# Kernel optimization log

Hardware: AMD Instinct MI355X
Metric: run time of the kernel (lower is better)

The kernel has to match this reference:

```python
import jax, jax.numpy as jnp
import numpy as np

DIM = 1024
HEADS = 16
HEAD_DIM = DIM // HEADS
B, N = 4, 4096


def setup_inputs() -> dict:
    key = jax.random.key(0)
    ks = jax.random.split(key, 10)
    s = 1.0 / np.sqrt(DIM)
    return {
        "x": jax.random.normal(ks[0], (B, N, DIM), dtype=jnp.float32),
        "Wq": jax.random.uniform(ks[1], (DIM, DIM), jnp.float32, -s, s),
        "bq": jax.random.uniform(ks[2], (DIM,), jnp.float32, -s, s),
        "Wk": jax.random.uniform(ks[3], (DIM, DIM), jnp.float32, -s, s),
        "bk": jax.random.uniform(ks[4], (DIM,), jnp.float32, -s, s),
        "Wv": jax.random.uniform(ks[5], (DIM, DIM), jnp.float32, -s, s),
        "bv": jax.random.uniform(ks[6], (DIM,), jnp.float32, -s, s),
        "Wo": jax.random.uniform(ks[7], (DIM, DIM), jnp.float32, -s, s),
        "bo": jax.random.uniform(ks[8], (DIM,), jnp.float32, -s, s),
        "stdp": jnp.ones((HEADS,), dtype=jnp.float32),
    }


def reference(x, Wq, bq, Wk, bk, Wv, bv, Wo, bo, stdp):
    b, n, d = x.shape
    h, dh = HEADS, HEAD_DIM
    # projections (torch Linear: x @ W.T + b)
    def proj(W, bias):
        return (x @ W.T + bias).reshape(b, n, h, dh).transpose(0, 2, 1, 3)  # bhnd
    Q = jax.nn.elu(proj(Wq, bq)) + 1.0
    K = jax.nn.elu(proj(Wk, bk)) + 1.0
    V = proj(Wv, bv)
    stdp_w = jax.nn.sigmoid(stdp).reshape(1, h, 1, 1)
    KV = jnp.einsum('bhnd,bhnv->bhdv', K, V)      # (b,h,dh,dh)
    K_sum = K.sum(axis=2)                          # (b,h,dh)
    numerator = jnp.einsum('bhnd,bhdv->bhnv', Q, KV)
    denominator = jnp.einsum('bhnd,bhd->bhn', Q, K_sum)[..., None] + 1e-6
    attn_out = numerator / denominator * stdp_w    # (b,h,n,dh)
    out = attn_out.transpose(0, 2, 1, 3).reshape(b, n, d)
    out = out @ Wo.T + bo
    return (out, jax.lax.stop_gradient(stdp))
```

## Files before the change

kernel.cpp:

```cpp
#include <hip/hip_runtime.h>
#include <hip/hip_bf16.h>

#define DIMSZ 1024
#define SEQLEN 4096
#define NHEAD 16
#define NX 16777216L
#define NW 1048576L

typedef __attribute__((ext_vector_type(8))) short bf16x8;
typedef __attribute__((ext_vector_type(4))) float f32x4;

__device__ __forceinline__ unsigned short f2bf(float f) {
    union { float f; unsigned int i; } c; c.f = f;
    unsigned int x = c.i;
    unsigned int r = (x + 0x7fffu + ((x >> 16) & 1u)) >> 16;
    return (unsigned short)r;
}

__device__ __forceinline__ unsigned int pk2(float lo, float hi) {
    union { float f; unsigned int i; } a, b; a.f = lo; b.f = hi;
    return __builtin_amdgcn_perm(b.i + 0x8000u, a.i + 0x8000u, 0x07060302u);
}

__device__ __forceinline__ void unp8r(bf16x8 v, float* f) {
    union { bf16x8 s; uint4 w; } u; u.s = v;
    union { unsigned int i; float f; } c;
    c.i = u.w.x << 16;           f[0] = c.f;
    c.i = u.w.x & 0xffff0000u;   f[1] = c.f;
    c.i = u.w.y << 16;           f[2] = c.f;
    c.i = u.w.y & 0xffff0000u;   f[3] = c.f;
    c.i = u.w.z << 16;           f[4] = c.f;
    c.i = u.w.z & 0xffff0000u;   f[5] = c.f;
    c.i = u.w.w << 16;           f[6] = c.f;
    c.i = u.w.w & 0xffff0000u;   f[7] = c.f;
}

__device__ __forceinline__ void async16(const void* g, void* l) {
    __builtin_amdgcn_global_load_lds(
        (const __attribute__((address_space(1))) void*)g,
        (__attribute__((address_space(3))) void*)l,
        16, 0, 0);
}

__global__ __launch_bounds__(256) void cast_pack(
    const float* __restrict__ x, const float* __restrict__ Wq,
    const float* __restrict__ Wk, const float* __restrict__ Wv,
    const float* __restrict__ Wo, const float* __restrict__ stdp,
    unsigned short* __restrict__ xb, unsigned short* __restrict__ Wqkv,
    unsigned short* __restrict__ Wob, float* __restrict__ outTail)
{
    long i4 = ((long)blockIdx.x * 256 + threadIdx.x) * 4;
    const float* src; unsigned short* dst; long off;
    if (i4 < NX)               { src = x;  dst = xb;          off = i4; }
    else if (i4 < NX + NW)     { src = Wq; dst = Wqkv;        off = i4 - NX; }
    else if (i4 < NX + 2*NW)   { src = Wk; dst = Wqkv + NW;   off = i4 - NX - NW; }
    else if (i4 < NX + 3*NW)   { src = Wv; dst = Wqkv + 2*NW; off = i4 - NX - 2*NW; }
    else                       { src = Wo; dst = Wob;         off = i4 - NX - 3*NW; }
    float4 v = *(const float4*)(src + off);
    union { unsigned short u[4]; uint2 p; } o;
    o.u[0] = f2bf(v.x); o.u[1] = f2bf(v.y); o.u[2] = f2bf(v.z); o.u[3] = f2bf(v.w);
    *(uint2*)(dst + off) = o.p;
    if (blockIdx.x == 0 && threadIdx.x < NHEAD) outTail[threadIdx.x] = stdp[threadIdx.x];
}

__global__ __launch_bounds__(512, 2) void qkv_gemm8(
    const unsigned short* __restrict__ A, const unsigned short* __restrict__ W,
    const float* __restrict__ bq, const float* __restrict__ bk,
    const float* __restrict__ bv,
    unsigned short* __restrict__ Qb, unsigned short* __restrict__ Kb,
    unsigned short* __restrict__ Vb)
{
    __shared__ __align__(16) char SM[131072];
    const int t = threadIdx.x;
    const int wave = t >> 6, lane = t & 63;
    const int lr = lane & 15, lq = lane >> 4;
    const int wm = wave >> 2, wn = wave & 3;
    const int m0 = blockIdx.x * 256;
    const int c0 = blockIdx.y * 256;

    const int sc = (((t & 7) ^ ((t >> 3) & 7)) * 8);
    const unsigned short* pA = A + (long)(m0 + (t >> 3)) * DIMSZ + sc;
    const unsigned short* pB = W + (long)(c0 + (t >> 3)) * DIMSZ + sc;
    char* ldsW = SM + wave * 1024;

    const int xo = ((lq ^ (lr & 7)) << 4);
    const char* ABase = SM + wm * 16384 + lr * 128;
    const char* BBase = SM + 32768 + (wn * 64 + lr) * 128;

    f32x4 acc[8][4];
    #pragma unroll
    for (int i = 0; i < 8; ++i)
        #pragma unroll
        for (int j = 0; j < 4; ++j) acc[i][j] = (f32x4){0.f, 0.f, 0.f, 0.f};

#define STAGE(Q, O) do {                                                        \
        if ((Q) < 16) {                                                         \
            const int isB_ = ((O) < 2) ? 1 : 0;                                 \
            const int half_ = isB_ ? (O) : ((O) - 2);                           \
            const unsigned short* s_ = (isB_ ? pB : pA)                         \
                                       + (long)half_ * 131072 + (Q) * 64;       \
            char* d_ = ldsW + (((Q) & 1) << 16) + isB_ * 32768 + half_ * 16384; \
            async16(s_, d_);                                                    \
            async16(s_ + 65536, d_ + 8192);                                     \
        }                                                                       \
    } while (0)

    STAGE(0, 0); STAGE(0, 1); STAGE(0, 2); STAGE(0, 3);
    STAGE(1, 0); STAGE(1, 1); STAGE(1, 2);
    asm volatile("s_waitcnt vmcnt(6)" ::: "memory");
    __builtin_amdgcn_s_barrier();

    for (int kt = 0; kt < 16; ++kt) {
        const int buf = (kt & 1) << 16;
        bf16x8 a0[4][2], a1[4][2], bfr[4][2];

        #pragma unroll
        for (int j = 0; j < 2; ++j) {
            bfr[j][0] = *(const bf16x8*)(BBase + buf + j * 2048 + xo);
            bfr[j][1] = *(const bf16x8*)(BBase + buf + j * 2048 + (xo ^ 64));
        }
        #pragma unroll
        for (int i = 0; i < 4; ++i) {
            a0[i][0] = *(const bf16x8*)(ABase + buf + i * 2048 + xo);
            a0[i][1] = *(const bf16x8*)(ABase + buf + i * 2048 + (xo ^ 64));
        }
        STAGE(kt + 1, 3);
        __builtin_amdgcn_s_barrier();
        asm volatile("s_waitcnt lgkmcnt(0)" ::: "memory");
        __builtin_amdgcn_sched_barrier(0);
        __builtin_amdgcn_s_setprio(1);
        #pragma unroll
        for (int s = 0; s < 2; ++s)
            #pragma unroll
            for (int i = 0; i < 4; ++i)
                #pragma unroll
                for (int j = 0; j < 2; ++j)
                    acc[i][j] = __builtin_amdgcn_mfma_f32_16x16x32_bf16(
                        bfr[j][s], a0[i][s], acc[i][j], 0, 0, 0);
        __builtin_amdgcn_s_setprio(0);
        __builtin_amdgcn_s_barrier();

        #pragma unroll
        for (int j = 2; j < 4; ++j) {
            bfr[j][0] = *(const bf16x8*)(BBase + buf + j * 2048 + xo);
            bfr[j][1] = *(const bf16x8*)(BBase + buf + j * 2048 + (xo ^ 64));
        }
        __builtin_amdgcn_s_barrier();
        asm volatile("s_waitcnt lgkmcnt(0)" ::: "memory");
        __builtin_amdgcn_sched_barrier(0);
        __builtin_amdgcn_s_setprio(1);
        #pragma unroll
        for (int s = 0; s < 2; ++s)
            #pragma unroll
            for (int i = 0; i < 4; ++i)
                #pragma unroll
                for (int j = 2; j < 4; ++j)
                    acc[i][j] = __builtin_amdgcn_mfma_f32_16x16x32_bf16(
                        bfr[j][s], a0[i][s], acc[i][j], 0, 0, 0);
        __builtin_amdgcn_s_setprio(0);
        __builtin_amdgcn_s_barrier();

        #pragma unroll
        for (int i = 0; i < 4; ++i) {
            a1[i][0] = *(const bf16x8*)(ABase + buf + (i + 4) * 2048 + xo);
            a1[i][1] = *(const bf16x8*)(ABase + buf + (i + 4) * 2048 + (xo ^ 64));
        }
        STAGE(kt + 2, 0);
        __builtin_amdgcn_s_barrier();
        asm volatile("s_waitcnt lgkmcnt(0)" ::: "memory");
        __builtin_amdgcn_sched_barrier(0);
        __builtin_amdgcn_s_setprio(1);
        #pragma unroll
        for (int s = 0; s < 2; ++s)
            #pragma unroll
            for (int i = 0; i < 4; ++i)
                #pragma unroll
                for (int j = 0; j < 2; ++j)
                    acc[i + 4][j] = __builtin_amdgcn_mfma_f32_16x16x32_bf16(
                        bfr[j][s], a1[i][s], acc[i + 4][j], 0, 0, 0);
        __builtin_amdgcn_s_setprio(0);
        __builtin_amdgcn_s_barrier();

        STAGE(kt + 2, 1);
        STAGE(kt + 2, 2);
        __builtin_amdgcn_s_barrier();
        __builtin_amdgcn_s_setprio(1);
        #pragma unroll
        for (int s = 0; s < 2; ++s)
            #pragma unroll
            for (int i = 0; i < 4; ++i)
                #pragma unroll
                for (int j = 2; j < 4; ++j)
                    acc[i + 4][j] = __builtin_amdgcn_mfma_f32_16x16x32_bf16(
                        bfr[j][s], a1[i][s], acc[i + 4][j], 0, 0, 0);
        __builtin_amdgcn_s_setprio(0);
        if (kt < 14)       asm volatile("s_waitcnt vmcnt(6)" ::: "memory");
        else if (kt == 14) asm volatile("s_waitcnt vmcnt(0)" ::: "memory");
        __builtin_amdgcn_s_barrier();
    }
#undef STAGE

    const int proj = c0 >> 10;
    const float* bias = proj == 0 ? bq : (proj == 1 ? bk : bv);
    const bool qk = proj < 2;
    const int cb = (c0 & 1023) + wn * 64;
    const int q4 = lq * 4;
    #pragma unroll
    for (int j = 0; j < 4; ++j) {
        const float4 b4 = *(const float4*)(bias + cb + 16 * j + q4);
        #pragma unroll
        for (int i = 0; i < 8; ++i) {
            float v0 = acc[i][j][0] + b4.x, v1 = acc[i][j][1] + b4.y;
            float v2 = acc[i][j][2] + b4.z, v3 = acc[i][j][3] + b4.w;
            if (qk) {
                v0 = v0 > 0.f ? v0 + 1.f : __expf(v0);
                v1 = v1 > 0.f ? v1 + 1.f : __expf(v1);
                v2 = v2 > 0.f ? v2 + 1.f : __expf(v2);
                v3 = v3 > 0.f ? v3 + 1.f : __expf(v3);
            }
            const int row = wm * 128 + 16 * i + lr;
            int byte = row * 512 + wn * 128 + j * 32 + q4 * 2;
            byte ^= (row & 7) << 4;
            uint2 pkd; pkd.x = pk2(v0, v1); pkd.y = pk2(v2, v3);
            *(uint2*)(SM + byte) = pkd;
        }
    }
    __syncthreads();
    unsigned short* dstp = proj == 0 ? Qb : (proj == 1 ? Kb : Vb);
    const int colsh = (t & 31) * 8;
    const int h = ((c0 >> 6) + (colsh >> 6)) & 15;
    const int b_ = m0 >> 12;
    unsigned short* dbase = dstp + ((long)(b_ * 16 + h) * SEQLEN) * 64 + (colsh & 63);
    #pragma unroll
    for (int u = 0; u < 16; ++u) {
        const int flat = u * 8192 + t * 16;
        const int row = flat >> 9;
        uint4 val = *(const uint4*)(SM + (flat ^ ((row & 7) << 4)));
        const int n = (m0 + row) & 4095;
        *(uint4*)(dbase + (long)n * 64) = val;
    }
}

__global__ __launch_bounds__(256) void kv_reduce(
    const unsigned short* __restrict__ Kb, const unsigned short* __restrict__ Vb,
    float* __restrict__ KVp, float* __restrict__ Ksump)
{
    __shared__ __align__(16) char LDS[65536];
    int bh = blockIdx.x, split = blockIdx.y, t = threadIdx.x;
    int wave = t >> 6, lane = t & 63, lr = lane & 15, lq = lane >> 4;

    const unsigned short* Kbase = Kb + ((long)bh * SEQLEN + split * 256) * 64;
    const unsigned short* Vbase = Vb + ((long)bh * SEQLEN + split * 256) * 64;

    const int nl = t & 127;
    const int dh = (t >> 7) * 32;

    union Q2S { uint4 q[4]; unsigned short s[32]; };
    Q2S kq[2], vq[2];
    #pragma unroll
    for (int it = 0; it < 2; ++it) {
        const unsigned short* kp = Kbase + (long)(it * 128 + nl) * 64 + dh;
        const unsigned short* vp = Vbase + (long)(it * 128 + nl) * 64 + dh;
        #pragma unroll
        for (int g = 0; g < 4; ++g) {
            kq[it].q[g] = *(const uint4*)(kp + g * 8);
            vq[it].q[g] = *(const uint4*)(vp + g * 8);
        }
    }
    #pragma unroll
    for (int it = 0; it < 2; ++it) {
        char* buf = LDS + it * 32768;
        #pragma unroll
        for (int e = 0; e < 32; ++e) {
            const int d = dh + e;
            const int a = d * 256 + ((nl * 2) ^ ((d & 7) << 4));
            *(unsigned short*)(buf + a) = kq[it].s[e];
            *(unsigned short*)(buf + 16384 + a) = vq[it].s[e];
        }
    }
    __syncthreads();

    f32x4 acc[4];
    #pragma unroll
    for (int j = 0; j < 4; ++j) acc[j] = (f32x4){0.f, 0.f, 0.f, 0.f};
    float ksp[4] = {0.f, 0.f, 0.f, 0.f};

    const int vrow = 16 * wave + lr;
    #pragma unroll
    for (int it = 0; it < 2; ++it) {
        const char* buf = LDS + it * 32768;
        #pragma unroll
        for (int ns = 0; ns < 4; ++ns) {
            const int xoff = (ns * 64 + lq * 16) ^ ((lr & 7) << 4);
            bf16x8 af = *(const bf16x8*)(buf + 16384 + vrow * 256 + xoff);
            bf16x8 bfr[4];
            #pragma unroll
            for (int j = 0; j < 4; ++j)
                bfr[j] = *(const bf16x8*)(buf + (16 * j + lr) * 256 + xoff);
            if (wave == 0) {
                #pragma unroll
                for (int j = 0; j < 4; ++j) {
                    float kf[8]; unp8r(bfr[j], kf);
                    ksp[j] += ((kf[0] + kf[1]) + (kf[2] + kf[3]))
                            + ((kf[4] + kf[5]) + (kf[6] + kf[7]));
                }
            }
            #pragma unroll
            for (int j = 0; j < 4; ++j)
                acc[j] = __builtin_amdgcn_mfma_f32_16x16x32_bf16(bfr[j], af, acc[j], 0, 0, 0);
        }
    }

    float* kp = KVp + ((long)split * 64 + bh) * 4096;
    const int q4 = lq * 4;
    #pragma unroll
    for (int j = 0; j < 4; ++j)
        *(f32x4*)(kp + vrow * 64 + 16 * j + q4) = acc[j];

    if (wave == 0) {
        #pragma unroll
        for (int j = 0; j < 4; ++j) {
            float s = ksp[j];
            s += __shfl_xor(s, 16);
            s += __shfl_xor(s, 32);
            if (lane < 16)
                Ksump[((long)split * 64 + bh) * 64 + 16 * j + lr] = s;
        }
    }
}

__global__ __launch_bounds__(256) void kv_final(
    const float* __restrict__ KVp, const float* __restrict__ Ksump,
    unsigned short* __restrict__ KVb, float* __restrict__ Ksum)
{
    int bh = blockIdx.x, t = threadIdx.x;
    float s[16];
    #pragma unroll
    for (int g = 0; g < 16; ++g) s[g] = 0.f;
    for (int sp = 0; sp < 16; ++sp) {
        const float* src = KVp + ((long)sp * 64 + bh) * 4096 + t * 16;
        #pragma unroll
        for (int g = 0; g < 4; ++g) {
            float4 v = *(const float4*)(src + g * 4);
            s[g * 4 + 0] += v.x; s[g * 4 + 1] += v.y;
            s[g * 4 + 2] += v.z; s[g * 4 + 3] += v.w;
        }
    }
    uint4 o0, o1;
    o0.x = pk2(s[0], s[1]);  o0.y = pk2(s[2], s[3]);
    o0.z = pk2(s[4], s[5]);  o0.w = pk2(s[6], s[7]);
    o1.x = pk2(s[8], s[9]);  o1.y = pk2(s[10], s[11]);
    o1.z = pk2(s[12], s[13]); o1.w = pk2(s[14], s[15]);
    *(uint4*)(KVb + (long)bh * 4096 + t * 16) = o0;
    *(uint4*)(KVb + (long)bh * 4096 + t * 16 + 8) = o1;
    if (t < 16) {
        float4 a = {0.f, 0.f, 0.f, 0.f};
        for (int p = 0; p < 16; p += 4) {
            #pragma unroll
            for (int q = 0; q < 4; ++q) {
                float4 v = *(const float4*)(Ksump + ((long)(p + q) * 64 + bh) * 64 + t * 4);
                a.x += v.x; a.y += v.y; a.z += v.z; a.w += v.w;
            }
        }
        *(float4*)(Ksum + bh * 64 + t * 4) = a;
    }
}

__global__ __launch_bounds__(256) void attn_kernel(
    const unsigned short* __restrict__ Qb, const unsigned short* __restrict__ KVb,
    const float* __restrict__ Ksum, const float* __restrict__ stdp,
    unsigned short* __restrict__ attn)
{
    __shared__ unsigned short Cs[256 * 72];
    int t = threadIdx.x;
    int rc = blockIdx.x;
    int bh = blockIdx.y;
    int b = bh >> 4, h = bh & 15;

    int wave = t >> 6, lane = t & 63, lr = lane & 15, lk = (lane >> 4) * 8;
    int rowbase = rc * 256 + wave * 64;
    const unsigned short* kvb = KVb + (long)bh * 4096;
    const float* ksb = Ksum + bh * 64;

    f32x4 acc[4][4];
    #pragma unroll
    for (int i = 0; i < 4; ++i)
        #pragma unroll
        for (int j = 0; j < 4; ++j) acc[i][j] = (f32x4){0.f, 0.f, 0.f, 0.f};
    float ds[4] = {0.f, 0.f, 0.f, 0.f};

    #pragma unroll
    for (int s0 = 0; s0 < 64; s0 += 32) {
        bf16x8 af[4], bfr[4];
        #pragma unroll
        for (int i = 0; i < 4; ++i)
            af[i] = *(const bf16x8*)(Qb + ((long)bh * SEQLEN + rowbase + 16 * i + lr) * 64 + s0 + lk);
        #pragma unroll
        for (int j = 0; j < 4; ++j)
            bfr[j] = *(const bf16x8*)(kvb + (16 * j + lr) * 64 + s0 + lk);
        float4 ka = *(const float4*)(ksb + s0 + lk);
        float4 kb2 = *(const float4*)(ksb + s0 + lk + 4);
        float ksf[8] = {ka.x, ka.y, ka.z, ka.w, kb2.x, kb2.y, kb2.z, kb2.w};
        #pragma unroll
        for (int i = 0; i < 4; ++i) {
            float qf[8]; unp8r(af[i], qf);
            #pragma unroll
            for (int e = 0; e < 8; ++e) ds[i] += qf[e] * ksf[e];
        }
        #pragma unroll
        for (int i = 0; i < 4; ++i)
            #pragma unroll
            for (int j = 0; j < 4; ++j)
                acc[i][j] = __builtin_amdgcn_mfma_f32_16x16x32_bf16(bfr[j], af[i], acc[i][j], 0, 0, 0);
    }

    float sg = 1.f / (1.f + __expf(-stdp[h]));
    float dinv_i[4];
    #pragma unroll
    for (int i = 0; i < 4; ++i) {
        float d = ds[i];
        d += __shfl_xor(d, 16);
        d += __shfl_xor(d, 32);
        dinv_i[i] = sg / (d + 1e-6f);
    }

    int q4 = (lane >> 4) * 4;
    #pragma unroll
    for (int j = 0; j < 4; ++j) {
        int v0c = 16 * j + q4;
        #pragma unroll
        for (int i = 0; i < 4; ++i) {
            int row = wave * 64 + 16 * i + lr;
            float d = dinv_i[i];
            uint2 pkd;
            pkd.x = pk2(acc[i][j][0] * d, acc[i][j][1] * d);
            pkd.y = pk2(acc[i][j][2] * d, acc[i][j][3] * d);
            *(uint2*)(Cs + row * 72 + v0c) = pkd;
        }
    }
    __syncthreads();
    #pragma unroll
    for (int u = 0; u < 8; ++u) {
        int row = u * 32 + (t >> 3);
        int nn = rc * 256 + row;
        long a = ((long)(b * SEQLEN + nn)) * DIMSZ + h * 64 + (t & 7) * 8;
        *(uint4*)(attn + a) = *(const uint4*)(Cs + row * 72 + (t & 7) * 8);
    }
}

__global__ __launch_bounds__(512, 2) void out_gemm8(
    const unsigned short* __restrict__ A, const unsigned short* __restrict__ W,
    const float* __restrict__ bo, float* __restrict__ out)
{
    __shared__ __align__(16) char SM[131072];
    const int t = threadIdx.x;
    const int wave = t >> 6, lane = t & 63;
    const int lr = lane & 15, lq = lane >> 4;
    const int wm = wave >> 2, wn = wave & 3;
    const int m0 = blockIdx.x * 256;
    const int c0 = blockIdx.y * 256;

    const int sc = (((t & 7) ^ ((t >> 3) & 7)) * 8);
    const unsigned short* pA = A + (long)(m0 + (t >> 3)) * DIMSZ + sc;
    const unsigned short* pB = W + (long)(c0 + (t >> 3)) * DIMSZ + sc;
    char* ldsW = SM + wave * 1024;

    const int xo = ((lq ^ (lr & 7)) << 4);
    const char* ABase = SM + wm * 16384 + lr * 128;
    const char* BBase = SM + 32768 + (wn * 64 + lr) * 128;

    f32x4 acc[8][4];
    #pragma unroll
    for (int i = 0; i < 8; ++i)
        #pragma unroll
        for (int j = 0; j < 4; ++j) acc[i][j] = (f32x4){0.f, 0.f, 0.f, 0.f};

#define STAGE(Q, O) do {                                                        \
        if ((Q) < 16) {                                                         \
            const int isB_ = ((O) < 2) ? 1 : 0;                                 \
            const int half_ = isB_ ? (O) : ((O) - 2);                           \
            const unsigned short* s_ = (isB_ ? pB : pA)                         \
                                       + (long)half_ * 131072 + (Q) * 64;       \
            char* d_ = ldsW + (((Q) & 1) << 16) + isB_ * 32768 + half_ * 16384; \
            async16(s_, d_);                                                    \
            async16(s_ + 65536, d_ + 8192);                                     \
        }                                                                       \
    } while (0)

    STAGE(0, 0); STAGE(0, 1); STAGE(0, 2); STAGE(0, 3);
    STAGE(1, 0); STAGE(1, 1); STAGE(1, 2);
    asm volatile("s_waitcnt vmcnt(6)" ::: "memory");
    __builtin_amdgcn_s_barrier();

    for (int kt = 0; kt < 16; ++kt) {
        const int buf = (kt & 1) << 16;
        bf16x8 a0[4][2], a1[4][2], bfr[4][2];

        #pragma unroll
        for (int j = 0; j < 2; ++j) {
            bfr[j][0] = *(const bf16x8*)(BBase + buf + j * 2048 + xo);
            bfr[j][1] = *(const bf16x8*)(BBase + buf + j * 2048 + (xo ^ 64));
        }
        #pragma unroll
        for (int i = 0; i < 4; ++i) {
            a0[i][0] = *(const bf16x8*)(ABase + buf + i * 2048 + xo);
            a0[i][1] = *(const bf16x8*)(ABase + buf + i * 2048 + (xo ^ 64));
        }
        STAGE(kt + 1, 3);
        __builtin_amdgcn_s_barrier();
        asm volatile("s_waitcnt lgkmcnt(0)" ::: "memory");
        __builtin_amdgcn_sched_barrier(0);
        __builtin_amdgcn_s_setprio(1);
        #pragma unroll
        for (int s = 0; s < 2; ++s)
            #pragma unroll
            for (int i = 0; i < 4; ++i)
                #pragma unroll
                for (int j = 0; j < 2; ++j)
                    acc[i][j] = __builtin_amdgcn_mfma_f32_16x16x32_bf16(
                        bfr[j][s], a0[i][s], acc[i][j], 0, 0, 0);
        __builtin_amdgcn_s_setprio(0);
        __builtin_amdgcn_s_barrier();

        #pragma unroll
        for (int j = 2; j < 4; ++j) {
            bfr[j][0] = *(const bf16x8*)(BBase + buf + j * 2048 + xo);
            bfr[j][1] = *(const bf16x8*)(BBase + buf + j * 2048 + (xo ^ 64));
        }
        __builtin_amdgcn_s_barrier();
        asm volatile("s_waitcnt lgkmcnt(0)" ::: "memory");
        __builtin_amdgcn_sched_barrier(0);
        __builtin_amdgcn_s_setprio(1);
        #pragma unroll
        for (int s = 0; s < 2; ++s)
            #pragma unroll
            for (int i = 0; i < 4; ++i)
                #pragma unroll
                for (int j = 2; j < 4; ++j)
                    acc[i][j] = __builtin_amdgcn_mfma_f32_16x16x32_bf16(
                        bfr[j][s], a0[i][s], acc[i][j], 0, 0, 0);
        __builtin_amdgcn_s_setprio(0);
        __builtin_amdgcn_s_barrier();

        #pragma unroll
        for (int i = 0; i < 4; ++i) {
            a1[i][0] = *(const bf16x8*)(ABase + buf + (i + 4) * 2048 + xo);
            a1[i][1] = *(const bf16x8*)(ABase + buf + (i + 4) * 2048 + (xo ^ 64));
        }
        STAGE(kt + 2, 0);
        __builtin_amdgcn_s_barrier();
        asm volatile("s_waitcnt lgkmcnt(0)" ::: "memory");
        __builtin_amdgcn_sched_barrier(0);
        __builtin_amdgcn_s_setprio(1);
        #pragma unroll
        for (int s = 0; s < 2; ++s)
            #pragma unroll
            for (int i = 0; i < 4; ++i)
                #pragma unroll
                for (int j = 0; j < 2; ++j)
                    acc[i + 4][j] = __builtin_amdgcn_mfma_f32_16x16x32_bf16(
                        bfr[j][s], a1[i][s], acc[i + 4][j], 0, 0, 0);
        __builtin_amdgcn_s_setprio(0);
        __builtin_amdgcn_s_barrier();

        STAGE(kt + 2, 1);
        STAGE(kt + 2, 2);
        __builtin_amdgcn_s_barrier();
        __builtin_amdgcn_s_setprio(1);
        #pragma unroll
        for (int s = 0; s < 2; ++s)
            #pragma unroll
            for (int i = 0; i < 4; ++i)
                #pragma unroll
                for (int j = 2; j < 4; ++j)
                    acc[i + 4][j] = __builtin_amdgcn_mfma_f32_16x16x32_bf16(
                        bfr[j][s], a1[i][s], acc[i + 4][j], 0, 0, 0);
        __builtin_amdgcn_s_setprio(0);
        if (kt < 14)       asm volatile("s_waitcnt vmcnt(6)" ::: "memory");
        else if (kt == 14) asm volatile("s_waitcnt vmcnt(0)" ::: "memory");
        __builtin_amdgcn_s_barrier();
    }
#undef STAGE

    const int q4 = lq * 4;
    #pragma unroll
    for (int j = 0; j < 4; ++j) {
        const int c = c0 + wn * 64 + 16 * j + q4;
        const float4 b4 = *(const float4*)(bo + c);
        #pragma unroll
        for (int i = 0; i < 8; ++i) {
            const int gm = m0 + wm * 128 + 16 * i + lr;
            float4 v;
            v.x = acc[i][j][0] + b4.x; v.y = acc[i][j][1] + b4.y;
            v.z = acc[i][j][2] + b4.z; v.w = acc[i][j][3] + b4.w;
            *(float4*)(out + (long)gm * DIMSZ + c) = v;
        }
    }
}

extern "C" void kernel_launch(void* const* d_in, const int* in_sizes, int n_in,
                              void* d_out, int out_size, void* d_ws, size_t ws_size,
                              hipStream_t stream) {
    const float* x    = (const float*)d_in[0];
    const float* Wq   = (const float*)d_in[1];
    const float* bq   = (const float*)d_in[2];
    const float* Wk   = (const float*)d_in[3];
    const float* bk   = (const float*)d_in[4];
    const float* Wv   = (const float*)d_in[5];
    const float* bv   = (const float*)d_in[6];
    const float* Wo   = (const float*)d_in[7];
    const float* bo   = (const float*)d_in[8];
    const float* stdp = (const float*)d_in[9];
    float* out = (float*)d_out;

    char* ws = (char*)d_ws;
    unsigned short* xb   = (unsigned short*)(ws);
    float*          KVp  = (float*)(ws);
    unsigned short* attn = (unsigned short*)(ws);
    unsigned short* Wqkv = (unsigned short*)(ws + 33554432L);
    float*          Ksump= (float*)(ws + 33554432L);
    unsigned short* KVb  = (unsigned short*)(ws + 33816576L);
    float*          Ksum = (float*)(ws + 34340864L);
    unsigned short* Wob  = (unsigned short*)(ws + 39845888L);
    unsigned short* Qb   = (unsigned short*)(ws + 41943040L);
    unsigned short* Kb   = (unsigned short*)(ws + 75497472L);
    unsigned short* Vb   = (unsigned short*)(ws + 109051904L);

    cast_pack<<<20480, 256, 0, stream>>>(x, Wq, Wk, Wv, Wo, stdp, xb, Wqkv, Wob,
                                         out + 16777216L);
    qkv_gemm8<<<dim3(64, 12), 512, 0, stream>>>(xb, Wqkv, bq, bk, bv, Qb, Kb, Vb);
    kv_reduce<<<dim3(64, 16), 256, 0, stream>>>(Kb, Vb, KVp, Ksump);
    kv_final<<<64, 256, 0, stream>>>(KVp, Ksump, KVb, Ksum);
    attn_kernel<<<dim3(16, 64), 256, 0, stream>>>(Qb, KVb, Ksum, stdp, attn);
    out_gemm8<<<dim3(64, 4), 512, 0, stream>>>(attn, Wob, bo, out);
}
```

Before: 323.8 us.

## Reschedule GEMM LDS loads, halve KV-reduce splits, and double attention rows per block

Both GEMM main loops now load all four B fragments up front and redistribute the global-to-LDS staging calls across phases, removing one barrier/wait pair per k-step. The KV reduction processes two 256-row chunks per block with half as many splits, so the final reduce sums fewer partials. The attention kernel keeps KV and Ksum fragments in registers and handles two row chunks per block, halving the grid. This trades register pressure and less parallelism for fewer barriers, less redundant loading and lower launch overhead.

```diff
diff --git a/kernel.cpp b/kernel.cpp
--- a/kernel.cpp
+++ b/kernel.cpp
@@ -6,6 +6,7 @@
 #define NHEAD 16
 #define NX 16777216L
 #define NW 1048576L
+#define KVSPLITS 8
 
 typedef __attribute__((ext_vector_type(8))) short bf16x8;
 typedef __attribute__((ext_vector_type(4))) float f32x4;
@@ -115,7 +116,7 @@
         bf16x8 a0[4][2], a1[4][2], bfr[4][2];
 
         #pragma unroll
-        for (int j = 0; j < 2; ++j) {
+        for (int j = 0; j < 4; ++j) {
             bfr[j][0] = *(const bf16x8*)(BBase + buf + j * 2048 + xo);
             bfr[j][1] = *(const bf16x8*)(BBase + buf + j * 2048 + (xo ^ 64));
         }
@@ -125,6 +126,7 @@
             a0[i][1] = *(const bf16x8*)(ABase + buf + i * 2048 + (xo ^ 64));
         }
         STAGE(kt + 1, 3);
+        asm volatile("s_waitcnt lgkmcnt(8)" ::: "memory");
         __builtin_amdgcn_s_barrier();
         asm volatile("s_waitcnt lgkmcnt(0)" ::: "memory");
         __builtin_amdgcn_sched_barrier(0);
@@ -140,14 +142,8 @@
         __builtin_amdgcn_s_setprio(0);
         __builtin_amdgcn_s_barrier();
 
-        #pragma unroll
-        for (int j = 2; j < 4; ++j) {
-            bfr[j][0] = *(const bf16x8*)(BBase + buf + j * 2048 + xo);
-            bfr[j][1] = *(const bf16x8*)(BBase + buf + j * 2048 + (xo ^ 64));
-        }
-        __builtin_amdgcn_s_barrier();
-        asm volatile("s_waitcnt lgkmcnt(0)" ::: "memory");
-        __builtin_amdgcn_sched_barrier(0);
+        STAGE(kt + 2, 0);
+        __builtin_amdgcn_s_barrier();
         __builtin_amdgcn_s_setprio(1);
         #pragma unroll
         for (int s = 0; s < 2; ++s)
@@ -165,7 +161,7 @@
             a1[i][0] = *(const bf16x8*)(ABase + buf + (i + 4) * 2048 + xo);
             a1[i][1] = *(const bf16x8*)(ABase + buf + (i + 4) * 2048 + (xo ^ 64));
         }
-        STAGE(kt + 2, 0);
+        STAGE(kt + 2, 1);
         __builtin_amdgcn_s_barrier();
         asm volatile("s_waitcnt lgkmcnt(0)" ::: "memory");
         __builtin_amdgcn_sched_barrier(0);
@@ -181,7 +177,6 @@
         __builtin_amdgcn_s_setprio(0);
         __builtin_amdgcn_s_barrier();
 
-        STAGE(kt + 2, 1);
         STAGE(kt + 2, 2);
         __builtin_amdgcn_s_barrier();
         __builtin_amdgcn_s_setprio(1);
@@ -249,65 +244,68 @@
     int bh = blockIdx.x, split = blockIdx.y, t = threadIdx.x;
     int wave = t >> 6, lane = t & 63, lr = lane & 15, lq = lane >> 4;
 
-    const unsigned short* Kbase = Kb + ((long)bh * SEQLEN + split * 256) * 64;
-    const unsigned short* Vbase = Vb + ((long)bh * SEQLEN + split * 256) * 64;
-
     const int nl = t & 127;
     const int dh = (t >> 7) * 32;
-
-    union Q2S { uint4 q[4]; unsigned short s[32]; };
-    Q2S kq[2], vq[2];
-    #pragma unroll
-    for (int it = 0; it < 2; ++it) {
-        const unsigned short* kp = Kbase + (long)(it * 128 + nl) * 64 + dh;
-        const unsigned short* vp = Vbase + (long)(it * 128 + nl) * 64 + dh;
-        #pragma unroll
-        for (int g = 0; g < 4; ++g) {
-            kq[it].q[g] = *(const uint4*)(kp + g * 8);
-            vq[it].q[g] = *(const uint4*)(vp + g * 8);
-        }
-    }
-    #pragma unroll
-    for (int it = 0; it < 2; ++it) {
-        char* buf = LDS + it * 32768;
-        #pragma unroll
-        for (int e = 0; e < 32; ++e) {
-            const int d = dh + e;
-            const int a = d * 256 + ((nl * 2) ^ ((d & 7) << 4));
-            *(unsigned short*)(buf + a) = kq[it].s[e];
-            *(unsigned short*)(buf + 16384 + a) = vq[it].s[e];
-        }
-    }
-    __syncthreads();
+    const int vrow = 16 * wave + lr;
 
     f32x4 acc[4];
     #pragma unroll
     for (int j = 0; j < 4; ++j) acc[j] = (f32x4){0.f, 0.f, 0.f, 0.f};
     float ksp[4] = {0.f, 0.f, 0.f, 0.f};
 
-    const int vrow = 16 * wave + lr;
-    #pragma unroll
-    for (int it = 0; it < 2; ++it) {
-        const char* buf = LDS + it * 32768;
-        #pragma unroll
-        for (int ns = 0; ns < 4; ++ns) {
-            const int xoff = (ns * 64 + lq * 16) ^ ((lr & 7) << 4);
-            bf16x8 af = *(const bf16x8*)(buf + 16384 + vrow * 256 + xoff);
-            bf16x8 bfr[4];
-            #pragma unroll
-            for (int j = 0; j < 4; ++j)
-                bfr[j] = *(const bf16x8*)(buf + (16 * j + lr) * 256 + xoff);
-            if (wave == 0) {
-                #pragma unroll
-                for (int j = 0; j < 4; ++j) {
-                    float kf[8]; unp8r(bfr[j], kf);
-                    ksp[j] += ((kf[0] + kf[1]) + (kf[2] + kf[3]))
-                            + ((kf[4] + kf[5]) + (kf[6] + kf[7]));
+    for (int half = 0; half < 2; ++half) {
+        const unsigned short* Kbase = Kb + ((long)bh * SEQLEN + split * 512 + half * 256) * 64;
+        const unsigned short* Vbase = Vb + ((long)bh * SEQLEN + split * 512 + half * 256) * 64;
+
+        union Q2S { uint4 q[4]; unsigned short s[32]; };
+        Q2S kq[2], vq[2];
+        #pragma unroll
+        for (int it = 0; it < 2; ++it) {
+            const unsigned short* kp = Kbase + (long)(it * 128 + nl) * 64 + dh;
+            const unsigned short* vp = Vbase + (long)(it * 128 + nl) * 64 + dh;
+            #pragma unroll
+            for (int g = 0; g < 4; ++g) {
+                kq[it].q[g] = *(const uint4*)(kp + g * 8);
+                vq[it].q[g] = *(const uint4*)(vp + g * 8);
+            }
+        }
+        if (half) __syncthreads();
+        #pragma unroll
+        for (int it = 0; it < 2; ++it) {
+            char* buf = LDS + it * 32768;
+            #pragma unroll
+            for (int e = 0; e < 32; ++e) {
+                const int d = dh + e;
+                const int a = d * 256 + ((nl * 2) ^ ((d & 7) << 4));
+                *(unsigned short*)(buf + a) = kq[it].s[e];
+                *(unsigned short*)(buf + 16384 + a) = vq[it].s[e];
+            }
+        }
+        __syncthreads();
+
+        #pragma unroll
+        for (int it = 0; it < 2; ++it) {
+            const char* buf = LDS + it * 32768;
+            #pragma unroll
+            for (int ns = 0; ns < 4; ++ns) {
+                const int xoff = (ns * 64 + lq * 16) ^ ((lr & 7) << 4);
+                bf16x8 af = *(const bf16x8*)(buf + 16384 + vrow * 256 + xoff);
+                bf16x8 bfr[4];
+                #pragma unroll
+                for (int j = 0; j < 4; ++j)
+                    bfr[j] = *(const bf16x8*)(buf + (16 * j + lr) * 256 + xoff);
+                if (wave == 0) {
+                    #pragma unroll
+                    for (int j = 0; j < 4; ++j) {
+                        float kf[8]; unp8r(bfr[j], kf);
+                        ksp[j] += ((kf[0] + kf[1]) + (kf[2] + kf[3]))
+                                + ((kf[4] + kf[5]) + (kf[6] + kf[7]));
+                    }
                 }
+                #pragma unroll
+                for (int j = 0; j < 4; ++j)
+                    acc[j] = __builtin_amdgcn_mfma_f32_16x16x32_bf16(bfr[j], af, acc[j], 0, 0, 0);
             }
-            #pragma unroll
-            for (int j = 0; j < 4; ++j)
-                acc[j] = __builtin_amdgcn_mfma_f32_16x16x32_bf16(bfr[j], af, acc[j], 0, 0, 0);
         }
     }
 
@@ -337,7 +335,7 @@
     float s[16];
     #pragma unroll
     for (int g = 0; g < 16; ++g) s[g] = 0.f;
-    for (int sp = 0; sp < 16; ++sp) {
+    for (int sp = 0; sp < KVSPLITS; ++sp) {
         const float* src = KVp + ((long)sp * 64 + bh) * 4096 + t * 16;
         #pragma unroll
         for (int g = 0; g < 4; ++g) {
@@ -355,7 +353,7 @@
     *(uint4*)(KVb + (long)bh * 4096 + t * 16 + 8) = o1;
     if (t < 16) {
         float4 a = {0.f, 0.f, 0.f, 0.f};
-        for (int p = 0; p < 16; p += 4) {
+        for (int p = 0; p < KVSPLITS; p += 4) {
             #pragma unroll
             for (int q = 0; q < 4; ++q) {
                 float4 v = *(const float4*)(Ksump + ((long)(p + q) * 64 + bh) * 64 + t * 4);
@@ -373,78 +371,89 @@
 {
     __shared__ unsigned short Cs[256 * 72];
     int t = threadIdx.x;
-    int rc = blockIdx.x;
     int bh = blockIdx.y;
     int b = bh >> 4, h = bh & 15;
 
     int wave = t >> 6, lane = t & 63, lr = lane & 15, lk = (lane >> 4) * 8;
-    int rowbase = rc * 256 + wave * 64;
     const unsigned short* kvb = KVb + (long)bh * 4096;
     const float* ksb = Ksum + bh * 64;
 
-    f32x4 acc[4][4];
-    #pragma unroll
-    for (int i = 0; i < 4; ++i)
-        #pragma unroll
-        for (int j = 0; j < 4; ++j) acc[i][j] = (f32x4){0.f, 0.f, 0.f, 0.f};
-    float ds[4] = {0.f, 0.f, 0.f, 0.f};
-
-    #pragma unroll
-    for (int s0 = 0; s0 < 64; s0 += 32) {
-        bf16x8 af[4], bfr[4];
+    bf16x8 bfrh[2][4];
+    float ksf[2][8];
+    #pragma unroll
+    for (int s = 0; s < 2; ++s) {
+        #pragma unroll
+        for (int j = 0; j < 4; ++j)
+            bfrh[s][j] = *(const bf16x8*)(kvb + (16 * j + lr) * 64 + s * 32 + lk);
+        float4 ka = *(const float4*)(ksb + s * 32 + lk);
+        float4 kb2 = *(const float4*)(ksb + s * 32 + lk + 4);
+        ksf[s][0] = ka.x; ksf[s][1] = ka.y; ksf[s][2] = ka.z; ksf[s][3] = ka.w;
+        ksf[s][4] = kb2.x; ksf[s][5] = kb2.y; ksf[s][6] = kb2.z; ksf[s][7] = kb2.w;
+    }
+    float sg = 1.f / (1.f + __expf(-stdp[h]));
+    int q4 = (lane >> 4) * 4;
+
+    for (int c = 0; c < 2; ++c) {
+        int rc = blockIdx.x * 2 + c;
+        int rowbase = rc * 256 + wave * 64;
+
+        f32x4 acc[4][4];
         #pragma unroll
         for (int i = 0; i < 4; ++i)
-            af[i] = *(const bf16x8*)(Qb + ((long)bh * SEQLEN + rowbase + 16 * i + lr) * 64 + s0 + lk);
-        #pragma unroll
-        for (int j = 0; j < 4; ++j)
-            bfr[j] = *(const bf16x8*)(kvb + (16 * j + lr) * 64 + s0 + lk);
-        float4 ka = *(const float4*)(ksb + s0 + lk);
-        float4 kb2 = *(const float4*)(ksb + s0 + lk + 4);
-        float ksf[8] = {ka.x, ka.y, ka.z, ka.w, kb2.x, kb2.y, kb2.z, kb2.w};
+            #pragma unroll
+            for (int j = 0; j < 4; ++j) acc[i][j] = (f32x4){0.f, 0.f, 0.f, 0.f};
+        float ds[4] = {0.f, 0.f, 0.f, 0.f};
+
+        #pragma unroll
+        for (int s = 0; s < 2; ++s) {
+            bf16x8 af[4];
+            #pragma unroll
+            for (int i = 0; i < 4; ++i)
+                af[i] = *(const bf16x8*)(Qb + ((long)bh * SEQLEN + rowbase + 16 * i + lr) * 64 + s * 32 + lk);
+            #pragma unroll
+            for (int i = 0; i < 4; ++i) {
+                float qf[8]; unp8r(af[i], qf);
+                #pragma unroll
+                for (int e = 0; e < 8; ++e) ds[i] += qf[e] * ksf[s][e];
+            }
+            #pragma unroll
+            for (int i = 0; i < 4; ++i)
+                #pragma unroll
+                for (int j = 0; j < 4; ++j)
+                    acc[i][j] = __builtin_amdgcn_mfma_f32_16x16x32_bf16(bfrh[s][j], af[i], acc[i][j], 0, 0, 0);
+        }
+
+        float dinv_i[4];
         #pragma unroll
         for (int i = 0; i < 4; ++i) {
-            float qf[8]; unp8r(af[i], qf);
-            #pragma unroll
-            for (int e = 0; e < 8; ++e) ds[i] += qf[e] * ksf[e];
-        }
-        #pragma unroll
-        for (int i = 0; i < 4; ++i)
-            #pragma unroll
-            for (int j = 0; j < 4; ++j)
-                acc[i][j] = __builtin_amdgcn_mfma_f32_16x16x32_bf16(bfr[j], af[i], acc[i][j], 0, 0, 0);
-    }
-
-    float sg = 1.f / (1.f + __expf(-stdp[h]));
-    float dinv_i[4];
-    #pragma unroll
-    for (int i = 0; i < 4; ++i) {
-        float d = ds[i];
-        d += __shfl_xor(d, 16);
-        d += __shfl_xor(d, 32);
-        dinv_i[i] = sg / (d + 1e-6f);
-    }
-
-    int q4 = (lane >> 4) * 4;
-    #pragma unroll
-    for (int j = 0; j < 4; ++j) {
-        int v0c = 16 * j + q4;
-        #pragma unroll
-        for (int i = 0; i < 4; ++i) {
-            int row = wave * 64 + 16 * i + lr;
-            float d = dinv_i[i];
-            uint2 pkd;
-            pkd.x = pk2(acc[i][j][0] * d, acc[i][j][1] * d);
-            pkd.y = pk2(acc[i][j][2] * d, acc[i][j][3] * d);
-            *(uint2*)(Cs + row * 72 + v0c) = pkd;
-        }
-    }
-    __syncthreads();
-    #pragma unroll
-    for (int u = 0; u < 8; ++u) {
-        int row = u * 32 + (t >> 3);
-        int nn = rc * 256 + row;
-        long a = ((long)(b * SEQLEN + nn)) * DIMSZ + h * 64 + (t & 7) * 8;
-        *(uint4*)(attn + a) = *(const uint4*)(Cs + row * 72 + (t & 7) * 8);
+            float d = ds[i];
+            d += __shfl_xor(d, 16);
+            d += __shfl_xor(d, 32);
+            dinv_i[i] = sg / (d + 1e-6f);
+        }
+
+        #pragma unroll
+        for (int j = 0; j < 4; ++j) {
+            int v0c = 16 * j + q4;
+            #pragma unroll
+            for (int i = 0; i < 4; ++i) {
+                int row = wave * 64 + 16 * i + lr;
+                float d = dinv_i[i];
+                uint2 pkd;
+                pkd.x = pk2(acc[i][j][0] * d, acc[i][j][1] * d);
+                pkd.y = pk2(acc[i][j][2] * d, acc[i][j][3] * d);
+                *(uint2*)(Cs + row * 72 + v0c) = pkd;
+            }
+        }
+        __syncthreads();
+        #pragma unroll
+        for (int u = 0; u < 8; ++u) {
+            int row = u * 32 + (t >> 3);
+            int nn = rc * 256 + row;
+            long a = ((long)(b * SEQLEN + nn)) * DIMSZ + h * 64 + (t & 7) * 8;
+            *(uint4*)(attn + a) = *(const uint4*)(Cs + row * 72 + (t & 7) * 8);
+        }
+        __syncthreads();
     }
 }
 
@@ -497,7 +506,7 @@
         bf16x8 a0[4][2], a1[4][2], bfr[4][2];
 
         #pragma unroll
-        for (int j = 0; j < 2; ++j) {
+        for (int j = 0; j < 4; ++j) {
             bfr[j][0] = *(const bf16x8*)(BBase + buf + j * 2048 + xo);
             bfr[j][1] = *(const bf16x8*)(BBase + buf + j * 2048 + (xo ^ 64));
         }
@@ -507,6 +516,7 @@
             a0[i][1] = *(const bf16x8*)(ABase + buf + i * 2048 + (xo ^ 64));
         }
         STAGE(kt + 1, 3);
+        asm volatile("s_waitcnt lgkmcnt(8)" ::: "memory");
         __builtin_amdgcn_s_barrier();
         asm volatile("s_waitcnt lgkmcnt(0)" ::: "memory");
         __builtin_amdgcn_sched_barrier(0);
@@ -522,14 +532,8 @@
         __builtin_amdgcn_s_setprio(0);
         __builtin_amdgcn_s_barrier();
 
-        #pragma unroll
-        for (int j = 2; j < 4; ++j) {
-            bfr[j][0] = *(const bf16x8*)(BBase + buf + j * 2048 + xo);
-            bfr[j][1] = *(const bf16x8*)(BBase + buf + j * 2048 + (xo ^ 64));
-        }
-        __builtin_amdgcn_s_barrier();
-        asm volatile("s_waitcnt lgkmcnt(0)" ::: "memory");
-        __builtin_amdgcn_sched_barrier(0);
+        STAGE(kt + 2, 0);
+        __builtin_amdgcn_s_barrier();
         __builtin_amdgcn_s_setprio(1);
         #pragma unroll
         for (int s = 0; s < 2; ++s)
@@ -547,7 +551,7 @@
             a1[i][0] = *(const bf16x8*)(ABase + buf + (i + 4) * 2048 + xo);
             a1[i][1] = *(const bf16x8*)(ABase + buf + (i + 4) * 2048 + (xo ^ 64));
         }
-        STAGE(kt + 2, 0);
+        STAGE(kt + 2, 1);
         __builtin_amdgcn_s_barrier();
         asm volatile("s_waitcnt lgkmcnt(0)" ::: "memory");
         __builtin_amdgcn_sched_barrier(0);
@@ -563,7 +567,6 @@
         __builtin_amdgcn_s_setprio(0);
         __builtin_amdgcn_s_barrier();
 
-        STAGE(kt + 2, 1);
         STAGE(kt + 2, 2);
         __builtin_amdgcn_s_barrier();
         __builtin_amdgcn_s_setprio(1);
@@ -629,8 +632,8 @@
     cast_pack<<<20480, 256, 0, stream>>>(x, Wq, Wk, Wv, Wo, stdp, xb, Wqkv, Wob,
                                          out + 16777216L);
     qkv_gemm8<<<dim3(64, 12), 512, 0, stream>>>(xb, Wqkv, bq, bk, bv, Qb, Kb, Vb);
-    kv_reduce<<<dim3(64, 16), 256, 0, stream>>>(Kb, Vb, KVp, Ksump);
+    kv_reduce<<<dim3(64, KVSPLITS), 256, 0, stream>>>(Kb, Vb, KVp, Ksump);
     kv_final<<<64, 256, 0, stream>>>(KVp, Ksump, KVb, Ksum);
-    attn_kernel<<<dim3(16, 64), 256, 0, stream>>>(Qb, KVb, Ksum, stdp, attn);
+    attn_kernel<<<dim3(8, 64), 256, 0, stream>>>(Qb, KVb, Ksum, stdp, attn);
     out_gemm8<<<dim3(64, 4), 512, 0, stream>>>(attn, Wob, bo, out);
 }
```

Measured after the change: 325.8 us. About the same (+0.6%).
